# Performance work log

Hardware: AMD Instinct MI355X
Metric: run time of the kernel (lower is better)

The kernel has to match this reference:

```python
import jax, jax.numpy as jnp
import numpy as np

B, S, D, DOUT = 8, 2048, 512, 512
BETA = 1.0
EPS = 1e-5


def _ln(x, g, b):
    m = jnp.mean(x, axis=-1, keepdims=True)
    v = jnp.var(x, axis=-1, keepdims=True)
    return (x - m) / jnp.sqrt(v + EPS) * g + b


def setup_inputs() -> dict:
    key = jax.random.key(0)
    ks = jax.random.split(key, 12)
    s = 0.02
    d = {
        "x": jax.random.normal(ks[0], (B, S, D), jnp.float32),
        "Wq": jax.random.normal(ks[1], (D, D), jnp.float32) * s,
        "bq": jnp.zeros((D,), jnp.float32),
        "Wk": jax.random.normal(ks[2], (D, D), jnp.float32) * s,
        "bk": jnp.zeros((D,), jnp.float32),
        "Wv": jax.random.normal(ks[3], (D, D), jnp.float32) * s,
        "bv": jnp.zeros((D,), jnp.float32),
        "ln0_g": jnp.ones((D,), jnp.float32),
        "ln0_b": jnp.zeros((D,), jnp.float32),
        "W1": jax.random.normal(ks[4], (D, D), jnp.float32) * s,
        "b1": jnp.zeros((D,), jnp.float32),
        "ln1_g": jnp.ones((D,), jnp.float32),
        "ln1_b": jnp.zeros((D,), jnp.float32),
        "W2": jax.random.normal(ks[5], (D, D), jnp.float32) * s,
        "b2": jnp.zeros((D,), jnp.float32),
        "ln2_g": jnp.ones((D,), jnp.float32),
        "ln2_b": jnp.zeros((D,), jnp.float32),
        "W3": jax.random.normal(ks[6], (D, DOUT), jnp.float32) * s,
        "b3": jnp.zeros((DOUT,), jnp.float32),
    }
    return d


def reference(x, Wq, bq, Wk, bk, Wv, bv, ln0_g, ln0_b,
              W1, b1, ln1_g, ln1_b, W2, b2, ln2_g, ln2_b, W3, b3):
    # --- attention_single (dropout disabled / eval) ---
    q = x @ Wq + bq                      # [B,S,D]
    k = x @ Wk + bk
    v = x @ Wv + bv
    scores = jnp.einsum('bsd,btd->bst', q, k)   # [B,S,S]
    w = jax.nn.softmax(BETA * scores / jnp.sqrt(jnp.float32(D)), axis=2)
    att = jnp.einsum('bst,btd->bsd', w, v)      # [B,S,D]
    out_nxt = _ln(x + att, ln0_g, ln0_b)
    # --- FFNN (dropout disabled, gelu activation) ---
    h1 = _ln(jax.nn.gelu(out_nxt + (out_nxt @ W1 + b1), approximate=False), ln1_g, ln1_b)
    h2 = _ln(jax.nn.gelu(out_nxt + (h1 @ W2 + b2), approximate=False), ln2_g, ln2_b)
    out_att = h2 @ W3 + b3               # [B,S,DOUT]
    return out_att
```

## Files before the change

kernel.cpp:

```cpp
#include <hip/hip_runtime.h>
#include <hip/hip_bf16.h>
#include <math.h>

using bf16 = __hip_bfloat16;
typedef __attribute__((ext_vector_type(8))) short short8;
typedef __attribute__((ext_vector_type(4))) float f32x4;
typedef __attribute__((ext_vector_type(4))) float float4v;

__device__ __forceinline__ float b2f(bf16 v) { return __bfloat162float(v); }
__device__ __forceinline__ bf16 f2b(float v) { return __float2bfloat16(v); }

__device__ __forceinline__ void gl_lds16(const bf16* g, bf16* l) {
  __builtin_amdgcn_global_load_lds(
      (const __attribute__((address_space(1))) void*)g,
      (__attribute__((address_space(3))) void*)l, 16, 0, 0);
}

__global__ __launch_bounds__(256) void sniff_zero(const void* ln0g_raw, int* flag,
                                                  float* rowsum) {
  const int i = blockIdx.x * 256 + threadIdx.x;
  rowsum[i] = 0.f;
  if (i == 0) {
    unsigned short w = ((const unsigned short*)ln0g_raw)[0];
    *flag = (w == 0x3F80) ? 1 : 0;
  }
}

__global__ __launch_bounds__(256) void conv_x8(
    const void* __restrict__ src, bf16* __restrict__ dst,
    const int* __restrict__ flag) {
  const long i = ((long)blockIdx.x * 256 + threadIdx.x) * 8;
  bf16 o[8];
  if (*flag) {
    *(short8*)(dst + i) = ((const short8*)src)[i >> 3];
  } else {
    float4v a = ((const float4v*)src)[i >> 2];
    float4v b = ((const float4v*)src)[(i >> 2) + 1];
#pragma unroll
    for (int k = 0; k < 4; k++) o[k] = f2b(a[k]);
#pragma unroll
    for (int k = 0; k < 4; k++) o[4 + k] = f2b(b[k]);
    *(short8*)(dst + i) = *(short8*)o;
  }
}

__global__ __launch_bounds__(256) void conv_vec12(
    const void* a0, const void* a1, const void* a2, const void* a3,
    const void* a4, const void* a5, const void* a6, const void* a7,
    const void* a8, const void* a9, const void* a10, const void* a11,
    bf16* __restrict__ dst, const int* __restrict__ flag) {
  const int j = blockIdx.x;
  const int i = threadIdx.x + (blockIdx.y << 8);
  const void* s;
  switch (j) {
    case 0: s = a0; break; case 1: s = a1; break; case 2: s = a2; break;
    case 3: s = a3; break; case 4: s = a4; break; case 5: s = a5; break;
    case 6: s = a6; break; case 7: s = a7; break; case 8: s = a8; break;
    case 9: s = a9; break; case 10: s = a10; break; default: s = a11; break;
  }
  bf16 v = (*flag) ? ((const bf16*)s)[i] : f2b(((const float*)s)[i]);
  dst[j * 512 + i] = v;
}

__global__ __launch_bounds__(256) void transpose_conv6(
    const void* w0, const void* w1, const void* w2, const void* w3,
    const void* w4, const void* w5, bf16* __restrict__ outBase,
    const int* __restrict__ flag) {
  __shared__ bf16 tile[32][33];
  const void* in;
  switch (blockIdx.z) {
    case 0: in = w0; break; case 1: in = w1; break; case 2: in = w2; break;
    case 3: in = w3; break; case 4: in = w4; break; default: in = w5; break;
  }
  bf16* out = outBase + (long)blockIdx.z * 262144;
  const int f = *flag;
  const int c0 = blockIdx.x * 32, r0 = blockIdx.y * 32;
  const int tx = threadIdx.x & 31, ty = threadIdx.x >> 5;
#pragma unroll
  for (int i = ty; i < 32; i += 8) {
    const long idx = (long)(r0 + i) * 512 + c0 + tx;
    tile[i][tx] = f ? ((const bf16*)in)[idx] : f2b(((const float*)in)[idx]);
  }
  __syncthreads();
#pragma unroll
  for (int i = ty; i < 32; i += 8)
    out[(long)(c0 + i) * 512 + r0 + tx] = tile[tx][i];
}

template <int EPI, bool BX>
__global__ __launch_bounds__(256, 2) void gemm_bt(
    const bf16* __restrict__ A, const bf16* __restrict__ Bt,
    const bf16* __restrict__ bias, const bf16* __restrict__ res,
    float* __restrict__ outF, bf16* __restrict__ outB,
    float* __restrict__ rowsum,
    int M, int N, int K, long sA, long sB, long sC, long sBias, float scale) {
  __shared__ __align__(16) bf16 As[128 * 32];
  __shared__ __align__(16) bf16 Bs[128 * 32];
  const int z = BX ? blockIdx.x : blockIdx.z;
  const int m0 = (BX ? blockIdx.y : blockIdx.x) * 128;
  const int n0 = (BX ? blockIdx.z : blockIdx.y) * 128;
  A += (long)z * sA;
  Bt += (long)z * sB;
  if (EPI == 0) bias += (long)z * sBias;
  const int t = threadIdx.x;
  const int l = t & 63, w = t >> 6;
  const int wm = (w >> 1) * 64, wn = (w & 1) * 64;
  const int lr = l & 15, lq = l >> 4;

  const bf16* Ab = A + (long)m0 * K;
  const bf16* Bb = Bt + (long)n0 * K;
  const int srow = t >> 2;
  const int scol = (t & 3) * 8;

  f32x4 acc[4][4] = {};

  for (int k0 = 0; k0 < K; k0 += 32) {
    gl_lds16(Ab + (long)srow * K + k0 + scol, As + w * 512);
    gl_lds16(Ab + (long)(srow + 64) * K + k0 + scol, As + 2048 + w * 512);
    gl_lds16(Bb + (long)srow * K + k0 + scol, Bs + w * 512);
    gl_lds16(Bb + (long)(srow + 64) * K + k0 + scol, Bs + 2048 + w * 512);
    __syncthreads();
    short8 af[4], bfr[4];
#pragma unroll
    for (int i = 0; i < 4; i++)
      af[i] = *(const short8*)(As + (wm + i * 16 + lr) * 32 + lq * 8);
#pragma unroll
    for (int j = 0; j < 4; j++)
      bfr[j] = *(const short8*)(Bs + (wn + j * 16 + lr) * 32 + lq * 8);
#pragma unroll
    for (int i = 0; i < 4; i++)
#pragma unroll
      for (int j = 0; j < 4; j++)
        acc[i][j] = __builtin_amdgcn_mfma_f32_16x16x32_bf16(af[i], bfr[j], acc[i][j], 0, 0, 0);
    __syncthreads();
  }

  const int cr = lq * 4, cc = lr;

  if (EPI == 1) {
    float rs[4][4];
#pragma unroll
    for (int i = 0; i < 4; i++)
#pragma unroll
      for (int r = 0; r < 4; r++) rs[i][r] = 0.f;
#pragma unroll
    for (int i = 0; i < 4; i++) {
#pragma unroll
      for (int j = 0; j < 4; j++) {
        const int gc = n0 + wn + j * 16 + cc;
#pragma unroll
        for (int r = 0; r < 4; r++) {
          const int gr = m0 + wm + i * 16 + cr + r;
          float e = __expf(acc[i][j][r] * scale);
          outB[(long)z * sC + (long)gr * N + gc] = f2b(e);
          rs[i][r] += e;
        }
      }
    }
#pragma unroll
    for (int o = 1; o < 16; o <<= 1)
#pragma unroll
      for (int i = 0; i < 4; i++)
#pragma unroll
        for (int r = 0; r < 4; r++) rs[i][r] += __shfl_xor(rs[i][r], o);
    if (lr == 0) {
#pragma unroll
      for (int i = 0; i < 4; i++)
#pragma unroll
        for (int r = 0; r < 4; r++) {
          const int gr = m0 + wm + i * 16 + cr + r;
          atomicAdd(&rowsum[(long)z * 2048 + gr], rs[i][r]);
        }
    }
    return;
  }

  float inv[4][4];
  if (EPI == 2) {
#pragma unroll
    for (int i = 0; i < 4; i++)
#pragma unroll
      for (int r = 0; r < 4; r++) {
        const int gr = m0 + wm + i * 16 + cr + r;
        inv[i][r] = 1.0f / rowsum[(long)z * 2048 + gr];
      }
  }

#pragma unroll
  for (int i = 0; i < 4; i++) {
#pragma unroll
    for (int j = 0; j < 4; j++) {
      const int gc = n0 + wn + j * 16 + cc;
#pragma unroll
      for (int r = 0; r < 4; r++) {
        const int gr = m0 + wm + i * 16 + cr + r;
        const long idx = (long)z * sC + (long)gr * N + gc;
        float v = acc[i][j][r];
        if (EPI == 0) {
          v += b2f(bias[gc]);
          outB[idx] = f2b(v);
        } else if (EPI == 2) {
          v = v * inv[i][r] + b2f(res[idx]);
          outB[idx] = f2b(v);
        } else if (EPI == 3) {
          v += b2f(bias[gc]) + b2f(res[idx]);
          v = 0.5f * v * (1.0f + erff(v * 0.70710678118654752f));
          outB[idx] = f2b(v);
        } else if (EPI == 4) {
          v += b2f(bias[gc]);
          outF[idx] = v;
        } else {
          v += b2f(bias[gr]);
          outB[idx] = f2b(v);
        }
      }
    }
  }
}

__global__ __launch_bounds__(256) void ln512(
    const bf16* __restrict__ mainb,
    const bf16* __restrict__ g, const bf16* __restrict__ b,
    bf16* __restrict__ out) {
  const long row = blockIdx.x;
  const int t = threadIdx.x;
  const long i0 = row * 512 + t, i1 = i0 + 256;
  float v0 = b2f(mainb[i0]);
  float v1 = b2f(mainb[i1]);
  float s = v0 + v1, q = v0 * v0 + v1 * v1;
#pragma unroll
  for (int o = 32; o > 0; o >>= 1) {
    s += __shfl_xor(s, o);
    q += __shfl_xor(q, o);
  }
  __shared__ float rs[4], rq[4];
  if ((t & 63) == 0) {
    rs[t >> 6] = s;
    rq[t >> 6] = q;
  }
  __syncthreads();
  s = (rs[0] + rs[1]) + (rs[2] + rs[3]);
  q = (rq[0] + rq[1]) + (rq[2] + rq[3]);
  const float mean = s * (1.f / 512.f);
  const float var = q * (1.f / 512.f) - mean * mean;
  const float rstd = rsqrtf(var + 1e-5f);
  out[i0] = f2b((v0 - mean) * rstd * b2f(g[t]) + b2f(b[t]));
  out[i1] = f2b((v1 - mean) * rstd * b2f(g[t + 256]) + b2f(b[t + 256]));
}

__global__ void sentinel_kernel(float* out) { out[0] = 31337.0f; }

extern "C" void kernel_launch(void* const* d_in, const int* in_sizes, int n_in,
                              void* d_out, int out_size, void* d_ws, size_t ws_size,
                              hipStream_t stream) {
  const void* x_raw = d_in[0];
  const void* Wq = d_in[1];
  const void* bq = d_in[2];
  const void* Wk = d_in[3];
  const void* bk = d_in[4];
  const void* Wv = d_in[5];
  const void* bv = d_in[6];
  const void* ln0g = d_in[7];
  const void* ln0b = d_in[8];
  const void* W1 = d_in[9];
  const void* b1 = d_in[10];
  const void* ln1g = d_in[11];
  const void* ln1b = d_in[12];
  const void* W2 = d_in[13];
  const void* b2 = d_in[14];
  const void* ln2g = d_in[15];
  const void* ln2b = d_in[16];
  const void* W3 = d_in[17];
  const void* b3 = d_in[18];

  const long MB = 1024 * 1024;
  if (ws_size < (size_t)(148 * MB)) {
    sentinel_kernel<<<1, 1, 0, stream>>>((float*)d_out);
    return;
  }
  char* ws = (char*)d_ws;
  bf16* Wqt = (bf16*)(ws + 0L * 524288);
  bf16* Wvt = (bf16*)(ws + 2L * 524288);
  bf16* W1t = (bf16*)(ws + 3L * 524288);
  bf16* W2t = (bf16*)(ws + 4L * 524288);
  bf16* W3t = (bf16*)(ws + 5L * 524288);
  int* flag = (int*)(ws + 3 * MB);
  bf16* vec = (bf16*)(ws + 3 * MB + 1024);
  bf16* bqc = vec + 0 * 512;
  bf16* bvc = vec + 2 * 512;
  bf16* ln0gc = vec + 3 * 512;
  bf16* ln0bc = vec + 4 * 512;
  bf16* b1c = vec + 5 * 512;
  bf16* ln1gc = vec + 6 * 512;
  bf16* ln1bc = vec + 7 * 512;
  bf16* b2c = vec + 8 * 512;
  bf16* ln2gc = vec + 9 * 512;
  bf16* ln2bc = vec + 10 * 512;
  bf16* b3c = vec + 11 * 512;
  float* rowsum = (float*)(ws + 3 * MB + 131072);
  bf16* xc = (bf16*)(ws + 4 * MB);
  bf16* qb = (bf16*)(ws + 20 * MB);
  bf16* kb = (bf16*)(ws + 36 * MB);
  bf16* vt = (bf16*)(ws + 52 * MB);
  bf16* sc = (bf16*)(ws + 68 * MB);
  bf16* sres = (bf16*)(ws + 132 * MB);
  bf16* onx = (bf16*)(ws + 20 * MB);
  bf16* preh = (bf16*)(ws + 68 * MB);
  bf16* h1 = (bf16*)(ws + 36 * MB);
  bf16* h2 = (bf16*)(ws + 100 * MB);

  const dim3 blk(256);
  const float scale = 0.044194173824159216f;
  const long sQ = 2048L * 512, sS = 2048L * 2048;

  sniff_zero<<<dim3(64), blk, 0, stream>>>(ln0g, flag, rowsum);
  conv_x8<<<dim3(4096), blk, 0, stream>>>(x_raw, xc, flag);
  conv_vec12<<<dim3(12, 2), blk, 0, stream>>>(bq, bk, bv, ln0g, ln0b, b1, ln1g,
                                              ln1b, b2, ln2g, ln2b, b3, vec, flag);
  transpose_conv6<<<dim3(16, 16, 6), blk, 0, stream>>>(Wq, Wk, Wv, W1, W2, W3,
                                                       Wqt, flag);

  gemm_bt<0, false><<<dim3(128, 4, 2), blk, 0, stream>>>(
      xc, Wqt, bqc, nullptr, nullptr, qb, nullptr,
      16384, 512, 512, 0, 262144, 8388608, 512, 1.f);
  gemm_bt<5, true><<<dim3(8, 4, 16), blk, 0, stream>>>(
      Wvt, xc, bvc, nullptr, nullptr, vt, nullptr,
      512, 2048, 512, 0, sQ, sQ, 0, 1.f);
  gemm_bt<1, true><<<dim3(8, 16, 16), blk, 0, stream>>>(
      qb, kb, nullptr, nullptr, nullptr, sc, rowsum,
      2048, 2048, 512, sQ, sQ, sS, 0, scale);
  gemm_bt<2, true><<<dim3(8, 16, 4), blk, 0, stream>>>(
      sc, vt, nullptr, xc, nullptr, sres, rowsum,
      2048, 512, 2048, sS, sQ, sQ, 0, 1.f);
  ln512<<<dim3(16384), blk, 0, stream>>>(sres, ln0gc, ln0bc, onx);
  gemm_bt<3, false><<<dim3(128, 4, 1), blk, 0, stream>>>(
      onx, W1t, b1c, onx, nullptr, preh, nullptr,
      16384, 512, 512, 0, 0, 0, 0, 1.f);
  ln512<<<dim3(16384), blk, 0, stream>>>(preh, ln1gc, ln1bc, h1);
  gemm_bt<3, false><<<dim3(128, 4, 1), blk, 0, stream>>>(
      h1, W2t, b2c, onx, nullptr, preh, nullptr,
      16384, 512, 512, 0, 0, 0, 0, 1.f);
  ln512<<<dim3(16384), blk, 0, stream>>>(preh, ln2gc, ln2bc, h2);
  gemm_bt<4, false><<<dim3(128, 4, 1), blk, 0, stream>>>(
      h2, W3t, b3c, nullptr, (float*)d_out, nullptr, nullptr,
      16384, 512, 512, 0, 0, 0, 0, 1.f);
}
```

Baseline: 379.3 us.

## Store softmax probabilities and V in FP8 and use FP8 MFMA for PV

The exponentiated scores and the transposed V projection are now written as e4m3 FP8 bytes instead of bf16, halving the dominant B*S*S score tensor's write and read traffic. A new FP8 GEMM kernel computes P·V with 16x16x32 fp8 MFMA and applies the row-sum normalization plus residual in its epilogue. Launch bounds are raised to 4 blocks per CU. This trades precision, since unnormalized exp values and V lose mantissa bits in e4m3, and could hurt accuracy.

Measured after the change: 375.8 us. No clear change (-0.9%).

```diff
diff --git a/kernel.cpp b/kernel.cpp
--- a/kernel.cpp
+++ b/kernel.cpp
@@ -10,7 +10,12 @@
 __device__ __forceinline__ float b2f(bf16 v) { return __bfloat162float(v); }
 __device__ __forceinline__ bf16 f2b(float v) { return __float2bfloat16(v); }
 
-__device__ __forceinline__ void gl_lds16(const bf16* g, bf16* l) {
+__device__ __forceinline__ unsigned char f2e4m3(float v) {
+  int p = __builtin_amdgcn_cvt_pk_fp8_f32(v, v, 0, false);
+  return (unsigned char)(p & 0xff);
+}
+
+__device__ __forceinline__ void gl_lds16(const void* g, void* l) {
   __builtin_amdgcn_global_load_lds(
       (const __attribute__((address_space(1))) void*)g,
       (__attribute__((address_space(3))) void*)l, 16, 0, 0);
@@ -88,11 +93,11 @@
 }
 
 template <int EPI, bool BX>
-__global__ __launch_bounds__(256, 2) void gemm_bt(
+__global__ __launch_bounds__(256, 4) void gemm_bt(
     const bf16* __restrict__ A, const bf16* __restrict__ Bt,
     const bf16* __restrict__ bias, const bf16* __restrict__ res,
     float* __restrict__ outF, bf16* __restrict__ outB,
-    float* __restrict__ rowsum,
+    unsigned char* __restrict__ out8, float* __restrict__ rowsum,
     int M, int N, int K, long sA, long sB, long sC, long sBias, float scale) {
   __shared__ __align__(16) bf16 As[128 * 32];
   __shared__ __align__(16) bf16 Bs[128 * 32];
@@ -152,7 +157,7 @@
         for (int r = 0; r < 4; r++) {
           const int gr = m0 + wm + i * 16 + cr + r;
           float e = __expf(acc[i][j][r] * scale);
-          outB[(long)z * sC + (long)gr * N + gc] = f2b(e);
+          out8[(long)z * sC + (long)gr * N + gc] = f2e4m3(e);
           rs[i][r] += e;
         }
       }
@@ -175,17 +180,6 @@
     return;
   }
 
-  float inv[4][4];
-  if (EPI == 2) {
-#pragma unroll
-    for (int i = 0; i < 4; i++)
-#pragma unroll
-      for (int r = 0; r < 4; r++) {
-        const int gr = m0 + wm + i * 16 + cr + r;
-        inv[i][r] = 1.0f / rowsum[(long)z * 2048 + gr];
-      }
-  }
-
 #pragma unroll
   for (int i = 0; i < 4; i++) {
 #pragma unroll
@@ -198,9 +192,6 @@
         float v = acc[i][j][r];
         if (EPI == 0) {
           v += b2f(bias[gc]);
-          outB[idx] = f2b(v);
-        } else if (EPI == 2) {
-          v = v * inv[i][r] + b2f(res[idx]);
           outB[idx] = f2b(v);
         } else if (EPI == 3) {
           v += b2f(bias[gc]) + b2f(res[idx]);
@@ -211,8 +202,75 @@
           outF[idx] = v;
         } else {
           v += b2f(bias[gr]);
-          outB[idx] = f2b(v);
+          out8[idx] = f2e4m3(v);
         }
+      }
+    }
+  }
+}
+
+__global__ __launch_bounds__(256, 4) void gemm_pv8(
+    const unsigned char* __restrict__ A8, const unsigned char* __restrict__ B8,
+    const bf16* __restrict__ res, bf16* __restrict__ outB,
+    const float* __restrict__ rowsum,
+    int M, int N, int K, long sA, long sB, long sC) {
+  __shared__ __align__(16) unsigned char As8[128 * 32];
+  __shared__ __align__(16) unsigned char Bs8[128 * 32];
+  const int z = blockIdx.x;
+  const int m0 = blockIdx.y * 128, n0 = blockIdx.z * 128;
+  A8 += (long)z * sA;
+  B8 += (long)z * sB;
+  const int t = threadIdx.x;
+  const int l = t & 63, w = t >> 6;
+  const int wm = (w >> 1) * 64, wn = (w & 1) * 64;
+  const int lr = l & 15, lq = l >> 4;
+
+  const unsigned char* Ab = A8 + (long)m0 * K;
+  const unsigned char* Bb = B8 + (long)n0 * K;
+  const int srow = t >> 1;
+  const int scol = (t & 1) * 16;
+
+  f32x4 acc[4][4] = {};
+
+  for (int k0 = 0; k0 < K; k0 += 32) {
+    gl_lds16(Ab + (long)srow * K + k0 + scol, As8 + w * 1024);
+    gl_lds16(Bb + (long)srow * K + k0 + scol, Bs8 + w * 1024);
+    __syncthreads();
+    long long a8[4], b8[4];
+#pragma unroll
+    for (int i = 0; i < 4; i++)
+      a8[i] = *(const long long*)(As8 + (wm + i * 16 + lr) * 32 + lq * 8);
+#pragma unroll
+    for (int j = 0; j < 4; j++)
+      b8[j] = *(const long long*)(Bs8 + (wn + j * 16 + lr) * 32 + lq * 8);
+#pragma unroll
+    for (int i = 0; i < 4; i++)
+#pragma unroll
+      for (int j = 0; j < 4; j++)
+        acc[i][j] = __builtin_amdgcn_mfma_f32_16x16x32_fp8_fp8(a8[i], b8[j], acc[i][j], 0, 0, 0);
+    __syncthreads();
+  }
+
+  const int cr = lq * 4, cc = lr;
+  float inv[4][4];
+#pragma unroll
+  for (int i = 0; i < 4; i++)
+#pragma unroll
+    for (int r = 0; r < 4; r++) {
+      const int gr = m0 + wm + i * 16 + cr + r;
+      inv[i][r] = 1.0f / rowsum[(long)z * 2048 + gr];
+    }
+#pragma unroll
+  for (int i = 0; i < 4; i++) {
+#pragma unroll
+    for (int j = 0; j < 4; j++) {
+      const int gc = n0 + wn + j * 16 + cc;
+#pragma unroll
+      for (int r = 0; r < 4; r++) {
+        const int gr = m0 + wm + i * 16 + cr + r;
+        const long idx = (long)z * sC + (long)gr * N + gc;
+        float v = acc[i][j][r] * inv[i][r] + b2f(res[idx]);
+        outB[idx] = f2b(v);
       }
     }
   }
@@ -301,8 +359,8 @@
   bf16* xc = (bf16*)(ws + 4 * MB);
   bf16* qb = (bf16*)(ws + 20 * MB);
   bf16* kb = (bf16*)(ws + 36 * MB);
-  bf16* vt = (bf16*)(ws + 52 * MB);
-  bf16* sc = (bf16*)(ws + 68 * MB);
+  unsigned char* vt8 = (unsigned char*)(ws + 52 * MB);
+  unsigned char* sc8 = (unsigned char*)(ws + 68 * MB);
   bf16* sres = (bf16*)(ws + 132 * MB);
   bf16* onx = (bf16*)(ws + 20 * MB);
   bf16* preh = (bf16*)(ws + 68 * MB);
@@ -321,27 +379,26 @@
                                                        Wqt, flag);
 
   gemm_bt<0, false><<<dim3(128, 4, 2), blk, 0, stream>>>(
-      xc, Wqt, bqc, nullptr, nullptr, qb, nullptr,
+      xc, Wqt, bqc, nullptr, nullptr, qb, nullptr, nullptr,
       16384, 512, 512, 0, 262144, 8388608, 512, 1.f);
-  gemm_bt<5, true><<<dim3(8, 4, 16), blk, 0, stream>>>(
-      Wvt, xc, bvc, nullptr, nullptr, vt, nullptr,
+  gemm_bt<6, true><<<dim3(8, 4, 16), blk, 0, stream>>>(
+      Wvt, xc, bvc, nullptr, nullptr, nullptr, vt8, nullptr,
       512, 2048, 512, 0, sQ, sQ, 0, 1.f);
   gemm_bt<1, true><<<dim3(8, 16, 16), blk, 0, stream>>>(
-      qb, kb, nullptr, nullptr, nullptr, sc, rowsum,
+      qb, kb, nullptr, nullptr, nullptr, nullptr, sc8, rowsum,
       2048, 2048, 512, sQ, sQ, sS, 0, scale);
-  gemm_bt<2, true><<<dim3(8, 16, 4), blk, 0, stream>>>(
-      sc, vt, nullptr, xc, nullptr, sres, rowsum,
-      2048, 512, 2048, sS, sQ, sQ, 0, 1.f);
+  gemm_pv8<<<dim3(8, 16, 4), blk, 0, stream>>>(
+      sc8, vt8, xc, sres, rowsum, 2048, 512, 2048, sS, sQ, sQ);
   ln512<<<dim3(16384), blk, 0, stream>>>(sres, ln0gc, ln0bc, onx);
   gemm_bt<3, false><<<dim3(128, 4, 1), blk, 0, stream>>>(
-      onx, W1t, b1c, onx, nullptr, preh, nullptr,
+      onx, W1t, b1c, onx, nullptr, preh, nullptr, nullptr,
       16384, 512, 512, 0, 0, 0, 0, 1.f);
   ln512<<<dim3(16384), blk, 0, stream>>>(preh, ln1gc, ln1bc, h1);
   gemm_bt<3, false><<<dim3(128, 4, 1), blk, 0, stream>>>(
-      h1, W2t, b2c, onx, nullptr, preh, nullptr,
+      h1, W2t, b2c, onx, nullptr, preh, nullptr, nullptr,
       16384, 512, 512, 0, 0, 0, 0, 1.f);
   ln512<<<dim3(16384), blk, 0, stream>>>(preh, ln2gc, ln2bc, h2);
   gemm_bt<4, false><<<dim3(128, 4, 1), blk, 0, stream>>>(
-      h2, W3t, b3c, nullptr, (float*)d_out, nullptr, nullptr,
+      h2, W3t, b3c, nullptr, (float*)d_out, nullptr, nullptr, nullptr,
       16384, 512, 512, 0, 0, 0, 0, 1.f);
 }
```
